# Performance work log

Hardware: AMD Instinct MI355X
Metric: run time of the kernel (lower is better)

The kernel has to match this reference:

```python
import jax, jax.numpy as jnp
import numpy as np
import math

VOCAB = 50000; D = 512; DEPTH = 6; N = 16; DCONV = 4; R = 32; DFF = 4 * D
B = 2; L = 1024

# A = -exp(A_log) with A_log = log(arange(1..N)) repeated over D  =>  A[d,n] = -(n+1)
A_CONT = -jnp.broadcast_to(jnp.arange(1.0, N + 1, dtype=jnp.float32), (D, N))


def sinusoidal(t, dim):
    half = dim // 2
    f = jnp.exp(jnp.arange(half, dtype=jnp.float32) * (-math.log(10000.0) / (half - 1)))
    e = t.astype(jnp.float32)[:, None] * f[None, :]
    return jnp.concatenate([jnp.sin(e), jnp.cos(e)], axis=-1)


def layernorm(x, g, b, eps=1e-5):
    mu = jnp.mean(x, -1, keepdims=True)
    var = jnp.mean((x - mu) ** 2, -1, keepdims=True)
    return (x - mu) * jax.lax.rsqrt(var + eps) * g + b


def ssm(x, Win, Wconv, Wdt, bdt, Dp, Wout):
    # x: [B,L,D]
    proj = x @ Win.T  # [B,L,2D+R+2N]
    xc, z, dtu, Bp, Cp = jnp.split(proj, [D, 2 * D, 2 * D + R, 2 * D + R + N], axis=-1)
    # depthwise causal conv (left pad d_conv-1 == pad both + truncate to L)
    conv = jax.lax.conv_general_dilated(
        xc.transpose(0, 2, 1), Wconv, (1,), [(DCONV - 1, 0)],
        dimension_numbers=('NCH', 'OIH', 'NCH'), feature_group_count=D)
    u = jax.nn.silu(conv.transpose(0, 2, 1))  # [B,L,D]
    dt = jax.nn.softplus(dtu @ Wdt.T + bdt)   # [B,L,D]
    At = jnp.exp(dt[..., None] * A_CONT)      # [B,L,D,N] (ZOH)
    Bu = ((At - 1.0) / (A_CONT + 1e-10)) * Bp[:, :, None, :] * u[..., None]  # [B,L,D,N]

    def step(h, xs):
        a, bu, c = xs
        h = a * h + bu                       # [B,D,N]
        return h, jnp.einsum('bn,bdn->bd', c, h)

    h0 = jnp.zeros((x.shape[0], D, N), dtype=x.dtype)
    _, ys = jax.lax.scan(step, h0, (At.transpose(1, 0, 2, 3), Bu.transpose(1, 0, 2, 3), Cp.transpose(1, 0, 2)))
    y = ys.transpose(1, 0, 2)                # [B,L,D]
    y = (y + u * Dp) * jax.nn.silu(z)
    return y @ Wout.T


def setup_inputs():
    key = jax.random.key(0)
    ks = iter(jax.random.split(key, 32))
    nrm = lambda shape: jax.random.normal(next(ks), shape, jnp.float32) * 0.02
    inp = {
        'x_t': jax.random.randint(next(ks), (B, L), 0, VOCAB + 1),
        't': jax.random.randint(next(ks), (B,), 0, 100),
        'tok_emb': nrm((VOCAB + 1, D)),
        'tmlp_w1': nrm((4 * D, D)), 'tmlp_b1': jnp.zeros((4 * D,)),
        'tmlp_w2': nrm((D, 4 * D)), 'tmlp_b2': jnp.zeros((D,)),
        'ln1_g': jnp.ones((DEPTH, D)), 'ln1_b': jnp.zeros((DEPTH, D)),
        'in_w': nrm((DEPTH, 2 * D + R + 2 * N, D)),
        'conv_w': nrm((DEPTH, D, 1, DCONV)),
        'dt_w': nrm((DEPTH, D, R)), 'dt_b': jnp.zeros((DEPTH, D)),
        'D_p': jnp.ones((DEPTH, D)),
        'out_w': nrm((DEPTH, D, D)),
        'ln2_g': jnp.ones((DEPTH, D)), 'ln2_b': jnp.zeros((DEPTH, D)),
        'mlp_w1': nrm((DEPTH, DFF, D)), 'mlp_b1': jnp.zeros((DEPTH, DFF)),
        'mlp_w2': nrm((DEPTH, D, DFF)), 'mlp_b2': jnp.zeros((DEPTH, D)),
        'lno_g': jnp.ones((D,)), 'lno_b': jnp.zeros((D,)),
        'head_w': nrm((VOCAB, D)), 'head_b': jnp.zeros((VOCAB,)),
    }
    return inp


def reference(x_t, t, tok_emb, tmlp_w1, tmlp_b1, tmlp_w2, tmlp_b2,
              ln1_g, ln1_b, in_w, conv_w, dt_w, dt_b, D_p, out_w,
              ln2_g, ln2_b, mlp_w1, mlp_b1, mlp_w2, mlp_b2,
              lno_g, lno_b, head_w, head_b):
    te = sinusoidal(t, D)
    te = jax.nn.silu(te @ tmlp_w1.T + tmlp_b1) @ tmlp_w2.T + tmlp_b2  # [B,D]
    x = tok_emb[x_t] + te[:, None, :]                                  # [B,L,D]
    for i in range(DEPTH):
        x = x + ssm(layernorm(x, ln1_g[i], ln1_b[i]),
                    in_w[i], conv_w[i], dt_w[i], dt_b[i], D_p[i], out_w[i])
        h = layernorm(x, ln2_g[i], ln2_b[i])
        x = x + jax.nn.gelu(h @ mlp_w1[i].T + mlp_b1[i], approximate=False) @ mlp_w2[i].T + mlp_b2[i]
    x = layernorm(x, lno_g, lno_b)
    return x @ head_w.T + head_b  # [B,L,VOCAB]
```

## Files before the change

kernel.cpp:

```cpp
#include <hip/hip_runtime.h>
#include <hip/hip_bf16.h>
#include <math.h>

typedef __hip_bfloat16 bf16;
typedef short s16x8 __attribute__((ext_vector_type(8)));
typedef float f32x4 __attribute__((ext_vector_type(4)));

#define M_TOK 2048
#define DD    512
#define LSEQ  1024
#define PW    1088
#define NST   16
#define RR    32
#define DFFW  2048
#define NCH   64
#define CH    16
#define PAD   36
#define NHEAD 50000
#define NHEADP 50048

__device__ __forceinline__ float bf2f(bf16 v) { return __bfloat162float(v); }
__device__ __forceinline__ float siluf(float x) { return x / (1.f + expf(-x)); }

__device__ __forceinline__ s16x8 cvt8(const f32x4& a, const f32x4& b) {
  s16x8 r;
  r[0] = (short)__bfloat16_as_ushort(__float2bfloat16(a[0]));
  r[1] = (short)__bfloat16_as_ushort(__float2bfloat16(a[1]));
  r[2] = (short)__bfloat16_as_ushort(__float2bfloat16(a[2]));
  r[3] = (short)__bfloat16_as_ushort(__float2bfloat16(a[3]));
  r[4] = (short)__bfloat16_as_ushort(__float2bfloat16(b[0]));
  r[5] = (short)__bfloat16_as_ushort(__float2bfloat16(b[1]));
  r[6] = (short)__bfloat16_as_ushort(__float2bfloat16(b[2]));
  r[7] = (short)__bfloat16_as_ushort(__float2bfloat16(b[3]));
  return r;
}

__device__ __forceinline__ void gload16(const bf16* g, bf16* l) {
  __builtin_amdgcn_global_load_lds((const __attribute__((address_space(1))) void*)g,
                                   (__attribute__((address_space(3))) void*)l, 16, 0, 0);
}

__constant__ float c_invn[NST] = {
  -1.f/1, -1.f/2, -1.f/3, -1.f/4, -1.f/5, -1.f/6, -1.f/7, -1.f/8,
  -1.f/9, -1.f/10, -1.f/11, -1.f/12, -1.f/13, -1.f/14, -1.f/15, -1.f/16 };

__global__ __launch_bounds__(256) void k_cvt(
    const float* __restrict__ src, bf16* __restrict__ dst, int n_src, int n_dst)
{
  for (int i = (blockIdx.x * 256 + threadIdx.x) * 8; i < n_dst; i += gridDim.x * 256 * 8) {
    s16x8 v;
    if (i + 8 <= n_src) {
      f32x4 a = *(const f32x4*)(src + i), b = *(const f32x4*)(src + i + 4);
      v = cvt8(a, b);
    } else {
      v = (s16x8){0,0,0,0,0,0,0,0};
    }
    *(s16x8*)((short*)dst + i) = v;
  }
}

__global__ __launch_bounds__(256) void k_te1(
    const int* __restrict__ t, const float* __restrict__ w1, const float* __restrict__ b1,
    float* __restrict__ h1)
{
  __shared__ float semb[2][512];
  int tid = threadIdx.x;
  float t0 = (float)t[0], t1 = (float)t[1];
  {
    int k = tid;
    float f = expf((float)k * (-9.210340371976184f / 255.f));
    semb[0][k]       = sinf(t0 * f);
    semb[0][k + 256] = cosf(t0 * f);
    semb[1][k]       = sinf(t1 * f);
    semb[1][k + 256] = cosf(t1 * f);
  }
  __syncthreads();
  int wave = tid >> 6, lane = tid & 63;
  int j = blockIdx.x * 4 + wave;
  const float* wr = w1 + (size_t)j * 512;
  float s0 = 0.f, s1 = 0.f;
#pragma unroll
  for (int i = 0; i < 8; ++i) {
    int k = lane + (i << 6);
    float wv = wr[k];
    s0 += wv * semb[0][k];
    s1 += wv * semb[1][k];
  }
  for (int o = 32; o; o >>= 1) { s0 += __shfl_down(s0, o); s1 += __shfl_down(s1, o); }
  if (!lane) {
    float bv = b1[j];
    h1[j]        = siluf(s0 + bv);
    h1[2048 + j] = siluf(s1 + bv);
  }
}

__global__ __launch_bounds__(256) void k_te2(
    const float* __restrict__ h1, const float* __restrict__ w2, const float* __restrict__ b2,
    float* __restrict__ te)
{
  __shared__ float sh1[2][2048];
  int tid = threadIdx.x;
  for (int idx = tid; idx < 4096; idx += 256)
    sh1[idx >> 11][idx & 2047] = h1[idx];
  __syncthreads();
  int wave = tid >> 6, lane = tid & 63;
  int d = blockIdx.x * 4 + wave;
  const float* wr = w2 + (size_t)d * 2048;
  float s0 = 0.f, s1 = 0.f;
#pragma unroll
  for (int i = 0; i < 32; ++i) {
    int k = lane + (i << 6);
    float wv = wr[k];
    s0 += wv * sh1[0][k];
    s1 += wv * sh1[1][k];
  }
  for (int o = 32; o; o >>= 1) { s0 += __shfl_down(s0, o); s1 += __shfl_down(s1, o); }
  if (!lane) {
    float bv = b2[d];
    te[d]       = s0 + bv;
    te[512 + d] = s1 + bv;
  }
}

__global__ __launch_bounds__(256) void k_embed(
    const int* __restrict__ x_t, const float* __restrict__ tok,
    const float* __restrict__ te, float* __restrict__ x)
{
  int m = blockIdx.x;
  int b = m >> 10;
  int row = x_t[m];
  const float* src = tok + (size_t)row * DD;
  for (int d = threadIdx.x; d < DD; d += 256)
    x[(size_t)m * DD + d] = src[d] + te[b * DD + d];
}

__global__ __launch_bounds__(256) void k_layernorm(
    const float* __restrict__ x, const float* __restrict__ g, const float* __restrict__ bb,
    bf16* __restrict__ out)
{
  int m = blockIdx.x;
  const float* xr = x + (size_t)m * DD;
  float2 v = ((const float2*)xr)[threadIdx.x];
  float s = v.x + v.y, ss = v.x * v.x + v.y * v.y;
  for (int o = 32; o; o >>= 1) { s += __shfl_down(s, o); ss += __shfl_down(ss, o); }
  __shared__ float ps[4], pss[4];
  int wave = threadIdx.x >> 6, lane = threadIdx.x & 63;
  if (!lane) { ps[wave] = s; pss[wave] = ss; }
  __syncthreads();
  s = ps[0] + ps[1] + ps[2] + ps[3];
  ss = pss[0] + pss[1] + pss[2] + pss[3];
  float mu = s * (1.f / DD);
  float var = ss * (1.f / DD) - mu * mu;
  float inv = rsqrtf(var + 1e-5f);
  int d = threadIdx.x * 2;
  out[(size_t)m * DD + d]     = __float2bfloat16((v.x - mu) * inv * g[d]     + bb[d]);
  out[(size_t)m * DD + d + 1] = __float2bfloat16((v.y - mu) * inv * g[d + 1] + bb[d + 1]);
}

__global__ __launch_bounds__(128) void k_scan1f(
    const float* __restrict__ proj, const float* __restrict__ convw,
    const float* __restrict__ dtw, const float* __restrict__ dtb,
    float* __restrict__ ubuf, float* __restrict__ yloc,
    float* __restrict__ Ebuf, float* __restrict__ Aprod, float* __restrict__ hend)
{
  int d = (blockIdx.x << 7) + threadIdx.x;
  int c = blockIdx.y, b = blockIdx.z;
  int m0 = b * LSEQ + c * CH;
  __shared__ float sBC[CH][32];
  __shared__ float sDT[CH][32];
  for (int idx = threadIdx.x; idx < CH * 32; idx += 128) {
    int l = idx >> 5, j = idx & 31;
    sBC[l][j] = proj[(size_t)(m0 + l) * PW + 2 * DD + RR + j];
    sDT[l][j] = proj[(size_t)(m0 + l) * PW + 2 * DD + j];
  }
  __syncthreads();
  float cw0 = convw[d * 4], cw1 = convw[d * 4 + 1], cw2 = convw[d * 4 + 2], cw3 = convw[d * 4 + 3];
  float dtbd = dtb[d];
  f32x4 wr[8];
#pragma unroll
  for (int i = 0; i < 8; ++i) wr[i] = *(const f32x4*)(dtw + (size_t)d * RR + i * 4);
  float w0 = 0.f, w1 = 0.f, w2 = 0.f;
  {
    int l0 = c * CH;
    if (l0 >= 3) w0 = proj[(size_t)(m0 - 3) * PW + d];
    if (l0 >= 2) w1 = proj[(size_t)(m0 - 2) * PW + d];
    if (l0 >= 1) w2 = proj[(size_t)(m0 - 1) * PW + d];
  }
  float h[NST];
#pragma unroll
  for (int n = 0; n < NST; ++n) h[n] = 0.f;
  float S = 0.f;
  for (int l = 0; l < CH; ++l) {
    size_t m = (size_t)(m0 + l);
    float xc = proj[m * PW + d];
    float cv = w0 * cw0 + w1 * cw1 + w2 * cw2 + xc * cw3;
    w0 = w1; w1 = w2; w2 = xc;
    float uv = siluf(cv);
    ubuf[m * DD + d] = uv;
    float s = dtbd;
#pragma unroll
    for (int i = 0; i < 8; ++i) {
      f32x4 q = *(const f32x4*)&sDT[l][i * 4];
      s += q[0] * wr[i][0] + q[1] * wr[i][1] + q[2] * wr[i][2] + q[3] * wr[i][3];
    }
    float dtv = (s > 0.f) ? (s + log1pf(expf(-s))) : log1pf(expf(s));
    float e1 = expf(-dtv);
    S += dtv;
    Ebuf[m * DD + d] = expf(-S);
    float p = 1.f, acc = 0.f;
#pragma unroll
    for (int n = 0; n < NST; ++n) {
      p *= e1;
      float bu = (p - 1.f) * c_invn[n] * sBC[l][n] * uv;
      h[n] = p * h[n] + bu;
      acc += sBC[l][16 + n] * h[n];
    }
    yloc[m * DD + d] = acc;
  }
  float Ec = expf(-S);
  float p = 1.f;
  size_t base = ((size_t)(b * NCH + c) * NST) * DD + d;
#pragma unroll
  for (int n = 0; n < NST; ++n) {
    p *= Ec;
    Aprod[base + (size_t)n * DD] = p;
    hend [base + (size_t)n * DD] = h[n];
  }
}

__global__ __launch_bounds__(256) void k_scan2(
    const float* __restrict__ Aprod, const float* __restrict__ hend, float* __restrict__ h0)
{
  int idx = blockIdx.x * 256 + threadIdx.x;
  int d = idx & 511;
  int n = (idx >> 9) & 15;
  int b = idx >> 13;
  float h = 0.f;
  for (int c = 0; c < NCH; ++c) {
    size_t o = ((size_t)((b * NCH + c) * NST + n)) * DD + d;
    h0[o] = h;
    h = Aprod[o] * h + hend[o];
  }
}

__global__ __launch_bounds__(128) void k_scan3(
    const float* __restrict__ proj, const float* __restrict__ u,
    const float* __restrict__ yloc, const float* __restrict__ Ebuf,
    const float* __restrict__ h0, const float* __restrict__ Dp, bf16* __restrict__ out)
{
  int d = (blockIdx.x << 7) + threadIdx.x;
  int c = blockIdx.y, b = blockIdx.z;
  int m0 = b * LSEQ + c * CH;
  __shared__ float sC[CH][NST];
  for (int idx = threadIdx.x; idx < CH * NST; idx += 128)
    sC[idx >> 4][idx & 15] = proj[(size_t)(m0 + (idx >> 4)) * PW + 2 * DD + RR + NST + (idx & 15)];
  __syncthreads();
  float hh[NST];
  size_t base = ((size_t)(b * NCH + c) * NST) * DD + d;
#pragma unroll
  for (int n = 0; n < NST; ++n) hh[n] = h0[base + (size_t)n * DD];
  float dpv = Dp[d];
  for (int l = 0; l < CH; ++l) {
    size_t m = (size_t)(m0 + l);
    float E = Ebuf[m * DD + d];
    float p = 1.f, corr = 0.f;
#pragma unroll
    for (int n = 0; n < NST; ++n) {
      p *= E;
      corr += sC[l][n] * p * hh[n];
    }
    float y = yloc[m * DD + d] + corr;
    float z = proj[m * PW + DD + d];
    float v = (y + u[m * DD + d] * dpv) * siluf(z);
    out[m * DD + d] = __float2bfloat16(v);
  }
}

template<int ACT, bool BF16OUT, bool RES, bool BIAS>
__global__ __launch_bounds__(256) void gemm_bb128(
    const bf16* __restrict__ A, const bf16* __restrict__ B,
    const float* __restrict__ bias, const float* __restrict__ res,
    void* __restrict__ Cout, int N, int K)
{
  __shared__ bf16 sA[2][128 * 32];
  __shared__ bf16 sB[2][128 * 32];
  int flat = blockIdx.y * gridDim.x + blockIdx.x;
  int qq = (gridDim.x * gridDim.y) >> 3;
  int s = (flat & 7) * qq + (flat >> 3);
  int bm = (s % gridDim.x) * 128;
  int bn = (s / gridDim.x) * 128;
  int tid = threadIdx.x;
  int wave = tid >> 6, lane = tid & 63;
  int wm = (wave >> 1) << 6, wn = (wave & 1) << 6;
  int r = lane & 15, q = lane >> 4;
  int srow = (wave << 4) + (lane >> 2);
  int scol = (lane & 3) << 3;
  const bf16* pA = A + (size_t)(bm + srow) * K + scol;
  const bf16* pB = B + (size_t)(bn + srow) * K + scol;
  int lbase = (wave << 4) << 5;

  f32x4 acc[4][4];
#pragma unroll
  for (int i = 0; i < 4; ++i)
#pragma unroll
    for (int j = 0; j < 4; ++j) acc[i][j] = (f32x4){0.f, 0.f, 0.f, 0.f};

  gload16(pA,                  sA[0] + lbase);
  gload16(pA + (size_t)64 * K, sA[0] + lbase + 64 * 32);
  gload16(pB,                  sB[0] + lbase);
  gload16(pB + (size_t)64 * K, sB[0] + lbase + 64 * 32);
  pA += 32; pB += 32;
  __syncthreads();

  int cur = 0;
  for (int k0 = 0; k0 < K; k0 += 32) {
    if (k0 + 32 < K) {
      gload16(pA,                  sA[cur ^ 1] + lbase);
      gload16(pA + (size_t)64 * K, sA[cur ^ 1] + lbase + 64 * 32);
      gload16(pB,                  sB[cur ^ 1] + lbase);
      gload16(pB + (size_t)64 * K, sB[cur ^ 1] + lbase + 64 * 32);
      pA += 32; pB += 32;
    }
    s16x8 af[4], bg[4];
#pragma unroll
    for (int i = 0; i < 4; ++i) af[i] = *(s16x8*)&sA[cur][((wm + i * 16 + r) << 5) + (q << 3)];
#pragma unroll
    for (int j = 0; j < 4; ++j) bg[j] = *(s16x8*)&sB[cur][((wn + j * 16 + r) << 5) + (q << 3)];
#pragma unroll
    for (int i = 0; i < 4; ++i)
#pragma unroll
      for (int j = 0; j < 4; ++j)
        acc[i][j] = __builtin_amdgcn_mfma_f32_16x16x32_bf16(af[i], bg[j], acc[i][j], 0, 0, 0);
    if (k0 + 32 < K) {
      __syncthreads();
      cur ^= 1;
    }
  }

#pragma unroll
  for (int i = 0; i < 4; ++i)
#pragma unroll
    for (int j = 0; j < 4; ++j) {
      int n = bn + wn + j * 16 + r;
      if (n >= N) continue;
#pragma unroll
      for (int e = 0; e < 4; ++e) {
        int m = bm + wm + i * 16 + (q << 2) + e;
        float v = acc[i][j][e];
        if (BIAS) v += bias[n];
        if (ACT == 1) v = 0.5f * v * (1.f + erff(v * 0.70710678118f));
        if (RES) v += res[(size_t)m * N + n];
        if (BF16OUT) ((bf16*)Cout)[(size_t)m * N + n] = __float2bfloat16(v);
        else         ((float*)Cout)[(size_t)m * N + n] = v;
      }
    }
}

template<int ACT, bool BF16OUT, bool RES, bool BIAS>
__global__ __launch_bounds__(256) void gemm_bb64(
    const bf16* __restrict__ A, const bf16* __restrict__ B,
    const float* __restrict__ bias, const float* __restrict__ res,
    void* __restrict__ Cout, int N, int K)
{
  __shared__ bf16 sA[2][64 * 32];
  __shared__ bf16 sB[2][64 * 32];
  int flat = blockIdx.y * gridDim.x + blockIdx.x;
  int qq = (gridDim.x * gridDim.y) >> 3;
  int s = (flat & 7) * qq + (flat >> 3);
  int bm = (s % gridDim.x) * 64;
  int bn = (s / gridDim.x) * 64;
  int tid = threadIdx.x;
  int wave = tid >> 6, lane = tid & 63;
  int wm = (wave >> 1) << 5, wn = (wave & 1) << 5;
  int r = lane & 15, q = lane >> 4;
  int srow = (wave << 4) + (lane >> 2);
  int scol = (lane & 3) << 3;
  const bf16* pA = A + (size_t)(bm + srow) * K + scol;
  const bf16* pB = B + (size_t)(bn + srow) * K + scol;
  int lbase = (wave << 4) << 5;

  f32x4 acc[2][2];
#pragma unroll
  for (int i = 0; i < 2; ++i)
#pragma unroll
    for (int j = 0; j < 2; ++j) acc[i][j] = (f32x4){0.f, 0.f, 0.f, 0.f};

  gload16(pA, sA[0] + lbase);
  gload16(pB, sB[0] + lbase);
  pA += 32; pB += 32;
  __syncthreads();

  int cur = 0;
  for (int k0 = 0; k0 < K; k0 += 32) {
    if (k0 + 32 < K) {
      gload16(pA, sA[cur ^ 1] + lbase);
      gload16(pB, sB[cur ^ 1] + lbase);
      pA += 32; pB += 32;
    }
    s16x8 af[2], bg[2];
#pragma unroll
    for (int i = 0; i < 2; ++i) af[i] = *(s16x8*)&sA[cur][((wm + i * 16 + r) << 5) + (q << 3)];
#pragma unroll
    for (int j = 0; j < 2; ++j) bg[j] = *(s16x8*)&sB[cur][((wn + j * 16 + r) << 5) + (q << 3)];
#pragma unroll
    for (int i = 0; i < 2; ++i)
#pragma unroll
      for (int j = 0; j < 2; ++j)
        acc[i][j] = __builtin_amdgcn_mfma_f32_16x16x32_bf16(af[i], bg[j], acc[i][j], 0, 0, 0);
    if (k0 + 32 < K) {
      __syncthreads();
      cur ^= 1;
    }
  }

#pragma unroll
  for (int i = 0; i < 2; ++i)
#pragma unroll
    for (int j = 0; j < 2; ++j) {
      int n = bn + wn + j * 16 + r;
#pragma unroll
      for (int e = 0; e < 4; ++e) {
        int m = bm + wm + i * 16 + (q << 2) + e;
        float v = acc[i][j][e];
        if (BIAS) v += bias[n];
        if (ACT == 1) v = 0.5f * v * (1.f + erff(v * 0.70710678118f));
        if (RES) v += res[(size_t)m * N + n];
        if (BF16OUT) ((bf16*)Cout)[(size_t)m * N + n] = __float2bfloat16(v);
        else         ((float*)Cout)[(size_t)m * N + n] = v;
      }
    }
}

template<int ACT, bool BF16OUT, bool RES, bool BIAS, bool SWZ>
__global__ __launch_bounds__(256) void gemm_abt(
    const bf16* __restrict__ A, const float* __restrict__ B,
    const float* __restrict__ bias, const float* __restrict__ res,
    void* __restrict__ Cout, int N, int K)
{
  __shared__ bf16 sA[128][PAD];
  __shared__ bf16 sB[128][PAD];
  int bn, bm;
  if (SWZ) {
    int flat = blockIdx.y * gridDim.x + blockIdx.x;
    int q = (gridDim.x * gridDim.y) >> 3;
    int s = (flat & 7) * q + (flat >> 3);
    bm = (s % gridDim.x) * 128;
    bn = (s / gridDim.x) * 128;
  } else {
    bn = blockIdx.x * 128;
    bm = blockIdx.y * 128;
  }
  int tid = threadIdx.x;
  int wave = tid >> 6, lane = tid & 63;
  int wm = (wave >> 1) << 6, wn = (wave & 1) << 6;
  int r = lane & 15, q = lane >> 4;
  int ldr = tid >> 2;
  int ldc = (tid & 3) << 3;
  f32x4 acc[4][4];
#pragma unroll
  for (int i = 0; i < 4; ++i)
#pragma unroll
    for (int j = 0; j < 4; ++j) acc[i][j] = (f32x4){0.f, 0.f, 0.f, 0.f};
  s16x8 pa[2];
  f32x4 pb[2][2];
#define GLOAD(k0)                                                              \
  {                                                                            \
    _Pragma("unroll")                                                          \
    for (int h = 0; h < 2; ++h) {                                              \
      int row = ldr + (h << 6);                                                \
      pa[h] = *(const s16x8*)(A + (size_t)(bm + row) * K + (k0) + ldc);        \
      int nrow = bn + row;                                                     \
      if (nrow < N) {                                                          \
        const float* src = B + (size_t)nrow * K + (k0) + ldc;                  \
        pb[h][0] = *(const f32x4*)src;                                         \
        pb[h][1] = *(const f32x4*)(src + 4);                                   \
      } else {                                                                 \
        pb[h][0] = (f32x4){0.f,0.f,0.f,0.f};                                   \
        pb[h][1] = (f32x4){0.f,0.f,0.f,0.f};                                   \
      }                                                                        \
    }                                                                          \
  }
  GLOAD(0);
  for (int k0 = 0; k0 < K; k0 += 32) {
#pragma unroll
    for (int h = 0; h < 2; ++h) {
      int row = ldr + (h << 6);
      *(s16x8*)&sA[row][ldc] = pa[h];
      *(s16x8*)&sB[row][ldc] = cvt8(pb[h][0], pb[h][1]);
    }
    __syncthreads();
    if (k0 + 32 < K) GLOAD(k0 + 32);
    s16x8 af[4], bg[4];
#pragma unroll
    for (int i = 0; i < 4; ++i) af[i] = *(s16x8*)&sA[wm + i * 16 + r][q << 3];
#pragma unroll
    for (int j = 0; j < 4; ++j) bg[j] = *(s16x8*)&sB[wn + j * 16 + r][q << 3];
#pragma unroll
    for (int i = 0; i < 4; ++i)
#pragma unroll
      for (int j = 0; j < 4; ++j)
        acc[i][j] = __builtin_amdgcn_mfma_f32_16x16x32_bf16(af[i], bg[j], acc[i][j], 0, 0, 0);
    __syncthreads();
  }
#undef GLOAD
#pragma unroll
  for (int i = 0; i < 4; ++i)
#pragma unroll
    for (int j = 0; j < 4; ++j) {
      int n = bn + wn + j * 16 + r;
      if (n >= N) continue;
#pragma unroll
      for (int e = 0; e < 4; ++e) {
        int m = bm + wm + i * 16 + (q << 2) + e;
        float v = acc[i][j][e];
        if (BIAS) v += bias[n];
        if (ACT == 1) v = 0.5f * v * (1.f + erff(v * 0.70710678118f));
        if (RES) v += res[(size_t)m * N + n];
        if (BF16OUT) ((bf16*)Cout)[(size_t)m * N + n] = __float2bfloat16(v);
        else         ((float*)Cout)[(size_t)m * N + n] = v;
      }
    }
}

template<int ACT, bool BF16OUT, bool RES, bool BIAS>
__global__ __launch_bounds__(256) void gemm64(
    const bf16* __restrict__ A, const float* __restrict__ B,
    const float* __restrict__ bias, const float* __restrict__ res,
    void* __restrict__ Cout, int N, int K)
{
  __shared__ bf16 sA[64][PAD];
  __shared__ bf16 sB[64][PAD];
  int bn = blockIdx.x * 64;
  int bm = blockIdx.y * 64;
  int tid = threadIdx.x;
  int wave = tid >> 6, lane = tid & 63;
  int wm = (wave >> 1) << 5, wn = (wave & 1) << 5;
  int r = lane & 15, q = lane >> 4;
  int ldr = tid >> 2;
  int ldc = (tid & 3) << 3;
  f32x4 acc[2][2];
#pragma unroll
  for (int i = 0; i < 2; ++i)
#pragma unroll
    for (int j = 0; j < 2; ++j) acc[i][j] = (f32x4){0.f, 0.f, 0.f, 0.f};
  s16x8 pa;
  f32x4 pb[2];
#define GLOAD64(k0)                                                            \
  {                                                                            \
    pa = *(const s16x8*)(A + (size_t)(bm + ldr) * K + (k0) + ldc);             \
    const float* src = B + (size_t)(bn + ldr) * K + (k0) + ldc;                \
    pb[0] = *(const f32x4*)src;                                                \
    pb[1] = *(const f32x4*)(src + 4);                                          \
  }
  GLOAD64(0);
  for (int k0 = 0; k0 < K; k0 += 32) {
    *(s16x8*)&sA[ldr][ldc] = pa;
    *(s16x8*)&sB[ldr][ldc] = cvt8(pb[0], pb[1]);
    __syncthreads();
    if (k0 + 32 < K) GLOAD64(k0 + 32);
    s16x8 af[2], bg[2];
#pragma unroll
    for (int i = 0; i < 2; ++i) af[i] = *(s16x8*)&sA[wm + i * 16 + r][q << 3];
#pragma unroll
    for (int j = 0; j < 2; ++j) bg[j] = *(s16x8*)&sB[wn + j * 16 + r][q << 3];
#pragma unroll
    for (int i = 0; i < 2; ++i)
#pragma unroll
      for (int j = 0; j < 2; ++j)
        acc[i][j] = __builtin_amdgcn_mfma_f32_16x16x32_bf16(af[i], bg[j], acc[i][j], 0, 0, 0);
    __syncthreads();
  }
#undef GLOAD64
#pragma unroll
  for (int i = 0; i < 2; ++i)
#pragma unroll
    for (int j = 0; j < 2; ++j) {
      int n = bn + wn + j * 16 + r;
#pragma unroll
      for (int e = 0; e < 4; ++e) {
        int m = bm + wm + i * 16 + (q << 2) + e;
        float v = acc[i][j][e];
        if (BIAS) v += bias[n];
        if (ACT == 1) v = 0.5f * v * (1.f + erff(v * 0.70710678118f));
        if (RES) v += res[(size_t)m * N + n];
        if (BF16OUT) ((bf16*)Cout)[(size_t)m * N + n] = __float2bfloat16(v);
        else         ((float*)Cout)[(size_t)m * N + n] = v;
      }
    }
}

extern "C" void kernel_launch(void* const* d_in, const int* in_sizes, int n_in,
                              void* d_out, int out_size, void* d_ws, size_t ws_size,
                              hipStream_t stream) {
  const int*   x_t     = (const int*)d_in[0];
  const int*   t       = (const int*)d_in[1];
  const float* tok_emb = (const float*)d_in[2];
  const float* tmlp_w1 = (const float*)d_in[3];
  const float* tmlp_b1 = (const float*)d_in[4];
  const float* tmlp_w2 = (const float*)d_in[5];
  const float* tmlp_b2 = (const float*)d_in[6];
  const float* ln1_g   = (const float*)d_in[7];
  const float* ln1_b   = (const float*)d_in[8];
  const float* in_w    = (const float*)d_in[9];
  const float* conv_w  = (const float*)d_in[10];
  const float* dt_w    = (const float*)d_in[11];
  const float* dt_b    = (const float*)d_in[12];
  const float* D_p     = (const float*)d_in[13];
  const float* out_w   = (const float*)d_in[14];
  const float* ln2_g   = (const float*)d_in[15];
  const float* ln2_b   = (const float*)d_in[16];
  const float* mlp_w1  = (const float*)d_in[17];
  const float* mlp_b1  = (const float*)d_in[18];
  const float* mlp_w2  = (const float*)d_in[19];
  const float* mlp_b2  = (const float*)d_in[20];
  const float* lno_g   = (const float*)d_in[21];
  const float* lno_b   = (const float*)d_in[22];
  const float* head_w  = (const float*)d_in[23];
  const float* head_b  = (const float*)d_in[24];

  char* w = (char*)d_ws;
  float* te    = (float*)w;  w += 4096;
  float* h1t   = (float*)w;  w += 16384;
  float* x     = (float*)w;  w += (size_t)M_TOK * DD * 4;
  bf16*  aIn   = (bf16*)w;   w += (size_t)M_TOK * DD * 2;
  float* proj  = (float*)w;  w += (size_t)M_TOK * PW * 4;
  float* ubuf  = (float*)w;  w += (size_t)M_TOK * DD * 4;
  float* ybuf  = (float*)w;  w += (size_t)M_TOK * DD * 4;
  float* Ebuf  = (float*)w;  w += (size_t)M_TOK * DD * 4;
  float* Aprod = (float*)w;  w += (size_t)2 * NCH * NST * DD * 4;
  float* hend  = (float*)w;  w += (size_t)2 * NCH * NST * DD * 4;
  float* h0    = (float*)w;  w += (size_t)2 * NCH * NST * DD * 4;
  bf16*  gbuf  = (bf16*)proj;
  bf16* bw_in   = (bf16*)w;  w += (size_t)6 * PW * DD * 2;
  bf16* bw_out  = (bf16*)w;  w += (size_t)6 * DD * DD * 2;
  bf16* bw_m1   = (bf16*)w;  w += (size_t)6 * DFFW * DD * 2;
  bf16* bw_m2   = (bf16*)w;  w += (size_t)6 * DD * DFFW * 2;
  bf16* bw_head = (bf16*)w;  w += (size_t)NHEADP * DD * 2;
  bool fast = ((size_t)(w - (char*)d_ws) <= ws_size);

  if (fast) {
    k_cvt<<<1024, 256, 0, stream>>>(in_w,   bw_in,   6 * PW * DD,   6 * PW * DD);
    k_cvt<<<1024, 256, 0, stream>>>(out_w,  bw_out,  6 * DD * DD,   6 * DD * DD);
    k_cvt<<<1024, 256, 0, stream>>>(mlp_w1, bw_m1,   6 * DFFW * DD, 6 * DFFW * DD);
    k_cvt<<<1024, 256, 0, stream>>>(mlp_w2, bw_m2,   6 * DD * DFFW, 6 * DD * DFFW);
    k_cvt<<<2048, 256, 0, stream>>>(head_w, bw_head, NHEAD * DD,    NHEADP * DD);
  }

  k_te1<<<512, 256, 0, stream>>>(t, tmlp_w1, tmlp_b1, h1t);
  k_te2<<<128, 256, 0, stream>>>(h1t, tmlp_w2, tmlp_b2, te);
  k_embed<<<M_TOK, 256, 0, stream>>>(x_t, tok_emb, te, x);

  for (int i = 0; i < 6; ++i) {
    const float* cw_i   = conv_w + (size_t)i * DD * 4;
    const float* dtw_i  = dt_w   + (size_t)i * DD * RR;
    const float* dtb_i  = dt_b   + (size_t)i * DD;
    const float* dp_i   = D_p    + (size_t)i * DD;
    const float* m1b_i  = mlp_b1 + (size_t)i * DFFW;
    const float* m2b_i  = mlp_b2 + (size_t)i * DD;

    k_layernorm<<<M_TOK, 256, 0, stream>>>(x, ln1_g + i * DD, ln1_b + i * DD, aIn);
    if (fast)
      gemm_bb64<0,false,false,false><<<dim3(M_TOK / 64, PW / 64), 256, 0, stream>>>(
          aIn, bw_in + (size_t)i * PW * DD, nullptr, nullptr, proj, PW, DD);
    else
      gemm64<0,false,false,false><<<dim3(PW / 64, M_TOK / 64), 256, 0, stream>>>(
          aIn, in_w + (size_t)i * PW * DD, nullptr, nullptr, proj, PW, DD);
    k_scan1f<<<dim3(4, NCH, 2), 128, 0, stream>>>(proj, cw_i, dtw_i, dtb_i,
                                                  ubuf, ybuf, Ebuf, Aprod, hend);
    k_scan2<<<2 * NST * DD / 256, 256, 0, stream>>>(Aprod, hend, h0);
    k_scan3<<<dim3(4, NCH, 2), 128, 0, stream>>>(proj, ubuf, ybuf, Ebuf, h0, dp_i, aIn);
    if (fast) {
      gemm_bb64<0,false,true,false><<<dim3(M_TOK / 64, DD / 64), 256, 0, stream>>>(
          aIn, bw_out + (size_t)i * DD * DD, nullptr, x, x, DD, DD);
      k_layernorm<<<M_TOK, 256, 0, stream>>>(x, ln2_g + i * DD, ln2_b + i * DD, aIn);
      gemm_bb128<1,true,false,true><<<dim3(M_TOK / 128, DFFW / 128), 256, 0, stream>>>(
          aIn, bw_m1 + (size_t)i * DFFW * DD, m1b_i, nullptr, gbuf, DFFW, DD);
      gemm_bb64<0,false,true,true><<<dim3(M_TOK / 64, DD / 64), 256, 0, stream>>>(
          gbuf, bw_m2 + (size_t)i * DD * DFFW, m2b_i, x, x, DD, DFFW);
    } else {
      gemm64<0,false,true,false><<<dim3(DD / 64, M_TOK / 64), 256, 0, stream>>>(
          aIn, out_w + (size_t)i * DD * DD, nullptr, x, x, DD, DD);
      k_layernorm<<<M_TOK, 256, 0, stream>>>(x, ln2_g + i * DD, ln2_b + i * DD, aIn);
      gemm64<1,true,false,true><<<dim3(DFFW / 64, M_TOK / 64), 256, 0, stream>>>(
          aIn, mlp_w1 + (size_t)i * DFFW * DD, m1b_i, nullptr, gbuf, DFFW, DD);
      gemm64<0,false,true,true><<<dim3(DD / 64, M_TOK / 64), 256, 0, stream>>>(
          gbuf, mlp_w2 + (size_t)i * DD * DFFW, m2b_i, x, x, DD, DFFW);
    }
  }

  k_layernorm<<<M_TOK, 256, 0, stream>>>(x, lno_g, lno_b, aIn);
  if (fast)
    gemm_bb128<0,false,false,true><<<dim3(M_TOK / 128, NHEADP / 128), 256, 0, stream>>>(
        aIn, bw_head, head_b, nullptr, d_out, NHEAD, DD);
  else
    gemm_abt<0,false,false,true,true><<<dim3(M_TOK / 128, (NHEAD + 127) / 128), 256, 0, stream>>>(
        aIn, head_w, head_b, nullptr, d_out, NHEAD, DD);
}
```

Baseline: 1.250 ms.

## Parallelize inter-chunk scan with wave shuffles, single-buffer GEMMs, smaller MLP1 tiles

The sequential 64-step inter-chunk carry scan is replaced by a Hillis-Steele prefix scan across the 64 lanes of a wavefront, using shuffles, one wave per (b,n,d) chain. Both bf16 GEMM kernels drop LDS double buffering for a single buffer with load, sync, compute, sync. This halves shared memory but removes the overlap of global loads with MFMA work. The MLP up-projection switches from 128x128 to 64x64 tiles, giving more blocks at the cost of reuse.

```diff
diff --git a/kernel.cpp b/kernel.cpp
--- a/kernel.cpp
+++ b/kernel.cpp
@@ -228,19 +228,24 @@
   }
 }
 
-__global__ __launch_bounds__(256) void k_scan2(
+__global__ __launch_bounds__(256) void k_scan2w(
     const float* __restrict__ Aprod, const float* __restrict__ hend, float* __restrict__ h0)
 {
-  int idx = blockIdx.x * 256 + threadIdx.x;
-  int d = idx & 511;
-  int n = (idx >> 9) & 15;
-  int b = idx >> 13;
-  float h = 0.f;
-  for (int c = 0; c < NCH; ++c) {
-    size_t o = ((size_t)((b * NCH + c) * NST + n)) * DD + d;
-    h0[o] = h;
-    h = Aprod[o] * h + hend[o];
-  }
+  int wave = threadIdx.x >> 6, lane = threadIdx.x & 63;
+  int chain = blockIdx.x * 4 + wave;
+  int d = chain & 511;
+  int n = (chain >> 9) & 15;
+  int b = chain >> 13;
+  size_t o = ((size_t)((b * NCH + lane) * NST + n)) * DD + d;
+  float A = Aprod[o], h = hend[o];
+#pragma unroll
+  for (int off = 1; off < 64; off <<= 1) {
+    float Ap = __shfl_up(A, off);
+    float hp = __shfl_up(h, off);
+    if (lane >= off) { h = A * hp + h; A = A * Ap; }
+  }
+  float hprev = __shfl_up(h, 1);
+  h0[o] = (lane == 0) ? 0.f : hprev;
 }
 
 __global__ __launch_bounds__(128) void k_scan3(
@@ -282,8 +287,8 @@
     const float* __restrict__ bias, const float* __restrict__ res,
     void* __restrict__ Cout, int N, int K)
 {
-  __shared__ bf16 sA[2][128 * 32];
-  __shared__ bf16 sB[2][128 * 32];
+  __shared__ bf16 sA[128 * 32];
+  __shared__ bf16 sB[128 * 32];
   int flat = blockIdx.y * gridDim.x + blockIdx.x;
   int qq = (gridDim.x * gridDim.y) >> 3;
   int s = (flat & 7) * qq + (flat >> 3);
@@ -297,7 +302,8 @@
   int scol = (lane & 3) << 3;
   const bf16* pA = A + (size_t)(bm + srow) * K + scol;
   const bf16* pB = B + (size_t)(bn + srow) * K + scol;
-  int lbase = (wave << 4) << 5;
+  bf16* lA = sA + ((wave << 4) << 5);
+  bf16* lB = sB + ((wave << 4) << 5);
 
   f32x4 acc[4][4];
 #pragma unroll
@@ -305,36 +311,24 @@
 #pragma unroll
     for (int j = 0; j < 4; ++j) acc[i][j] = (f32x4){0.f, 0.f, 0.f, 0.f};
 
-  gload16(pA,                  sA[0] + lbase);
-  gload16(pA + (size_t)64 * K, sA[0] + lbase + 64 * 32);
-  gload16(pB,                  sB[0] + lbase);
-  gload16(pB + (size_t)64 * K, sB[0] + lbase + 64 * 32);
-  pA += 32; pB += 32;
-  __syncthreads();
-
-  int cur = 0;
   for (int k0 = 0; k0 < K; k0 += 32) {
-    if (k0 + 32 < K) {
-      gload16(pA,                  sA[cur ^ 1] + lbase);
-      gload16(pA + (size_t)64 * K, sA[cur ^ 1] + lbase + 64 * 32);
-      gload16(pB,                  sB[cur ^ 1] + lbase);
-      gload16(pB + (size_t)64 * K, sB[cur ^ 1] + lbase + 64 * 32);
-      pA += 32; pB += 32;
-    }
+    gload16(pA,                  lA);
+    gload16(pA + (size_t)64 * K, lA + 64 * 32);
+    gload16(pB,                  lB);
+    gload16(pB + (size_t)64 * K, lB + 64 * 32);
+    pA += 32; pB += 32;
+    __syncthreads();
     s16x8 af[4], bg[4];
 #pragma unroll
-    for (int i = 0; i < 4; ++i) af[i] = *(s16x8*)&sA[cur][((wm + i * 16 + r) << 5) + (q << 3)];
-#pragma unroll
-    for (int j = 0; j < 4; ++j) bg[j] = *(s16x8*)&sB[cur][((wn + j * 16 + r) << 5) + (q << 3)];
+    for (int i = 0; i < 4; ++i) af[i] = *(s16x8*)&sA[((wm + i * 16 + r) << 5) + (q << 3)];
+#pragma unroll
+    for (int j = 0; j < 4; ++j) bg[j] = *(s16x8*)&sB[((wn + j * 16 + r) << 5) + (q << 3)];
 #pragma unroll
     for (int i = 0; i < 4; ++i)
 #pragma unroll
       for (int j = 0; j < 4; ++j)
         acc[i][j] = __builtin_amdgcn_mfma_f32_16x16x32_bf16(af[i], bg[j], acc[i][j], 0, 0, 0);
-    if (k0 + 32 < K) {
-      __syncthreads();
-      cur ^= 1;
-    }
+    __syncthreads();
   }
 
 #pragma unroll
@@ -362,8 +356,8 @@
     const float* __restrict__ bias, const float* __restrict__ res,
     void* __restrict__ Cout, int N, int K)
 {
-  __shared__ bf16 sA[2][64 * 32];
-  __shared__ bf16 sB[2][64 * 32];
+  __shared__ bf16 sA[64 * 32];
+  __shared__ bf16 sB[64 * 32];
   int flat = blockIdx.y * gridDim.x + blockIdx.x;
   int qq = (gridDim.x * gridDim.y) >> 3;
   int s = (flat & 7) * qq + (flat >> 3);
@@ -377,7 +371,8 @@
   int scol = (lane & 3) << 3;
   const bf16* pA = A + (size_t)(bm + srow) * K + scol;
   const bf16* pB = B + (size_t)(bn + srow) * K + scol;
-  int lbase = (wave << 4) << 5;
+  bf16* lA = sA + ((wave << 4) << 5);
+  bf16* lB = sB + ((wave << 4) << 5);
 
   f32x4 acc[2][2];
 #pragma unroll
@@ -385,32 +380,22 @@
 #pragma unroll
     for (int j = 0; j < 2; ++j) acc[i][j] = (f32x4){0.f, 0.f, 0.f, 0.f};
 
-  gload16(pA, sA[0] + lbase);
-  gload16(pB, sB[0] + lbase);
-  pA += 32; pB += 32;
-  __syncthreads();
-
-  int cur = 0;
   for (int k0 = 0; k0 < K; k0 += 32) {
-    if (k0 + 32 < K) {
-      gload16(pA, sA[cur ^ 1] + lbase);
-      gload16(pB, sB[cur ^ 1] + lbase);
-      pA += 32; pB += 32;
-    }
+    gload16(pA, lA);
+    gload16(pB, lB);
+    pA += 32; pB += 32;
+    __syncthreads();
     s16x8 af[2], bg[2];
 #pragma unroll
-    for (int i = 0; i < 2; ++i) af[i] = *(s16x8*)&sA[cur][((wm + i * 16 + r) << 5) + (q << 3)];
-#pragma unroll
-    for (int j = 0; j < 2; ++j) bg[j] = *(s16x8*)&sB[cur][((wn + j * 16 + r) << 5) + (q << 3)];
+    for (int i = 0; i < 2; ++i) af[i] = *(s16x8*)&sA[((wm + i * 16 + r) << 5) + (q << 3)];
+#pragma unroll
+    for (int j = 0; j < 2; ++j) bg[j] = *(s16x8*)&sB[((wn + j * 16 + r) << 5) + (q << 3)];
 #pragma unroll
     for (int i = 0; i < 2; ++i)
 #pragma unroll
       for (int j = 0; j < 2; ++j)
         acc[i][j] = __builtin_amdgcn_mfma_f32_16x16x32_bf16(af[i], bg[j], acc[i][j], 0, 0, 0);
-    if (k0 + 32 < K) {
-      __syncthreads();
-      cur ^= 1;
-    }
+    __syncthreads();
   }
 
 #pragma unroll
@@ -667,13 +652,13 @@
           aIn, in_w + (size_t)i * PW * DD, nullptr, nullptr, proj, PW, DD);
     k_scan1f<<<dim3(4, NCH, 2), 128, 0, stream>>>(proj, cw_i, dtw_i, dtb_i,
                                                   ubuf, ybuf, Ebuf, Aprod, hend);
-    k_scan2<<<2 * NST * DD / 256, 256, 0, stream>>>(Aprod, hend, h0);
+    k_scan2w<<<2 * NST * DD / 4, 256, 0, stream>>>(Aprod, hend, h0);
     k_scan3<<<dim3(4, NCH, 2), 128, 0, stream>>>(proj, ubuf, ybuf, Ebuf, h0, dp_i, aIn);
     if (fast) {
       gemm_bb64<0,false,true,false><<<dim3(M_TOK / 64, DD / 64), 256, 0, stream>>>(
           aIn, bw_out + (size_t)i * DD * DD, nullptr, x, x, DD, DD);
       k_layernorm<<<M_TOK, 256, 0, stream>>>(x, ln2_g + i * DD, ln2_b + i * DD, aIn);
-      gemm_bb128<1,true,false,true><<<dim3(M_TOK / 128, DFFW / 128), 256, 0, stream>>>(
+      gemm_bb64<1,true,false,true><<<dim3(M_TOK / 64, DFFW / 64), 256, 0, stream>>>(
           aIn, bw_m1 + (size_t)i * DFFW * DD, m1b_i, nullptr, gbuf, DFFW, DD);
       gemm_bb64<0,false,true,true><<<dim3(M_TOK / 64, DD / 64), 256, 0, stream>>>(
           gbuf, bw_m2 + (size_t)i * DD * DFFW, m2b_i, x, x, DD, DFFW);
```

After: 1.122 ms. -10.2%, faster.
